# Kernel tuning notes

Hardware: AMD Instinct MI355X
Metric: run time of the kernel (lower is better)

## Reference

```python
import jax, jax.numpy as jnp
import numpy as np

COMMITMENT_COST = 0.25


def setup_inputs() -> dict:
    key = jax.random.key(0)
    k1, k2 = jax.random.split(key)
    inputs = jax.random.normal(k1, (32, 64, 32, 32), dtype=jnp.float32)  # (B, C, H, W)
    embed = jax.random.normal(k2, (64, 1024), dtype=jnp.float32)          # (embedding_dim, num_embeddings)
    return {"inputs": inputs, "embed": embed}


def reference(inputs, embed):
    # Eval-mode forward (EMA buffer updates are training-only side effects).
    B, C, H, W = inputs.shape
    K = embed.shape[1]
    flat = inputs.transpose(0, 2, 3, 1).reshape(-1, C)  # (N, C)
    N = flat.shape[0]

    distances = (jnp.sum(flat * flat, axis=1, keepdims=True)
                 + jnp.sum(embed * embed, axis=0)
                 - 2.0 * flat @ embed)
    encoding_indices = jnp.argmin(distances, axis=1)  # (N,)

    # Gather instead of one-hot @ embed.T (same math, no N x K one-hot)
    quantized = embed.T[encoding_indices]  # (N, C)

    e_latent_loss = jnp.mean((jax.lax.stop_gradient(quantized) - flat) ** 2)
    loss = COMMITMENT_COST * e_latent_loss

    # straight-through estimator
    quantized_st = flat + jax.lax.stop_gradient(quantized - flat)
    quantized_out = quantized_st.reshape(B, H, W, C).transpose(0, 3, 1, 2)

    # avg_probs via scatter-add counts (== mean of one-hot encodings)
    counts = jnp.zeros((K,), dtype=flat.dtype).at[encoding_indices].add(1.0)
    avg_probs = counts / N
    perplexity = jnp.exp(-jnp.sum(avg_probs * jnp.log(avg_probs + 1e-10)))

    return quantized_out, loss, encoding_indices, perplexity
```

## Files before the change

kernel.cpp:

```cpp
#include <hip/hip_runtime.h>

#define N_PIX  32768
#define C_DIM  64
#define K_EMB  1024
#define HW     1024
#define PIXB   32

#define OUT_Q_OFF    0
#define OUT_LOSS_OFF 2097152
#define OUT_IDX_OFF  2097153
#define OUT_PERP_OFF 2129921

typedef __attribute__((ext_vector_type(8)))  __bf16 bf16x8;
typedef __attribute__((ext_vector_type(16))) float  f32x16;

__device__ unsigned short g_esplit[3 * K_EMB * C_DIM];
__device__ uint4          g_eesplit[2 * K_EMB];
__device__ float          g_ee[K_EMB];
__device__ unsigned int   g_counts[K_EMB];
__device__ float          g_lossAcc;

__device__ __forceinline__ unsigned short f2bf(float f) {
    unsigned u = __float_as_uint(f);
    unsigned r = u + 0x7FFFu + ((u >> 16) & 1u);
    return (unsigned short)(r >> 16);
}
__device__ __forceinline__ float bf2f(unsigned short b) {
    return __uint_as_float(((unsigned)b) << 16);
}
__device__ __forceinline__ unsigned long long pack_score(float d, int k) {
    unsigned int u = __float_as_uint(d);
    u = (u & 0x80000000u) ? ~u : (u | 0x80000000u);
    return ((unsigned long long)u << 32) | (unsigned int)k;
}
__device__ __forceinline__ uint4 pack8(const unsigned short* v) {
    uint4 u;
    u.x = (unsigned)v[0] | ((unsigned)v[1] << 16);
    u.y = (unsigned)v[2] | ((unsigned)v[3] << 16);
    u.z = (unsigned)v[4] | ((unsigned)v[5] << 16);
    u.w = (unsigned)v[6] | ((unsigned)v[7] << 16);
    return u;
}
__device__ __forceinline__ unsigned long long shfl_xor32_u64(unsigned long long v) {
    unsigned lo = (unsigned)v, hi = (unsigned)(v >> 32);
    lo = __shfl_xor(lo, 32, 64);
    hi = __shfl_xor(hi, 32, 64);
    return ((unsigned long long)hi << 32) | lo;
}
#define UPD2(P1, P2, MM) { \
    if ((MM) < P1) { P2 = P1; P1 = (MM); } else if ((MM) < P2) P2 = (MM); }
#define MRG2(P1, P2, O1, O2) { \
    unsigned long long _lo = (O1) < P1 ? (O1) : P1; \
    unsigned long long _hi = (O1) < P1 ? P1 : (O1); \
    unsigned long long _m2 = (O2) < P2 ? (O2) : P2; \
    P1 = _lo; P2 = _hi < _m2 ? _hi : _m2; }

__global__ void k_prep(const float* __restrict__ embed) {
    const int code = blockIdx.x * 64 + threadIdx.x;
    if (code == 0) g_lossAcc = 0.f;
    g_counts[code] = 0u;
    const int tile = code >> 5, c32 = code & 31;
    uint4* o = reinterpret_cast<uint4*>(g_esplit);
    float ee = 0.f;
#pragma unroll
    for (int s = 0; s < 4; ++s)
#pragma unroll
        for (int hh = 0; hh < 2; ++hh) {
            unsigned short b1[8], b2[8], b3[8];
#pragma unroll
            for (int e = 0; e < 8; ++e) {
                const float x = embed[(s * 16 + hh * 8 + e) * K_EMB + code];
                ee = fmaf(x, x, ee);
                b1[e] = f2bf(x);
                const float r1 = x - bf2f(b1[e]);
                b2[e] = f2bf(r1);
                const float r2 = r1 - bf2f(b2[e]);
                b3[e] = f2bf(r2);
            }
            const int oi = tile * 256 + s * 64 + hh * 32 + c32;
            o[oi        ] = pack8(b1);
            o[oi +  8192] = pack8(b2);
            o[oi + 16384] = pack8(b3);
        }
    g_ee[code] = ee;
    const float v = -0.5f * ee;
    const unsigned short e1 = f2bf(v);
    const float r1 = v - bf2f(e1);
    const unsigned short e2 = f2bf(r1);
    const float r2 = r1 - bf2f(e2);
    const unsigned short e3 = f2bf(r2);
    g_eesplit[code] = make_uint4((unsigned)e1 | ((unsigned)e2 << 16),
                                 (unsigned)e3, 0u, 0u);
    g_eesplit[K_EMB + code] = make_uint4(0u, 0u, 0u, 0u);
}

__global__ __launch_bounds__(256, 2) void k_main(
    const float* __restrict__ inp, const float* __restrict__ embed,
    float* __restrict__ out_q, float* __restrict__ out_idx) {

    __shared__ float x_raw[C_DIM * PIXB];
    __shared__ uint4 xfrag[3 * 4 * 2 * PIXB];
    __shared__ unsigned long long red1[4][PIXB];
    __shared__ unsigned long long red2[4][PIXB];
    __shared__ int   ksel[PIXB];
    __shared__ float lred[4];
    __shared__ float bdist;

    const int tid = threadIdx.x;
    const int n0  = blockIdx.x * PIXB;
    const int b   = n0 >> 10;
    const int hw0 = n0 & 1023;
    const float* __restrict__ xg = inp + b * (C_DIM * HW) + hw0;

#pragma unroll
    for (int i = 0; i < 2; ++i) {
        const int F = tid + i * 256;
        const int c = F >> 3, p4 = (F & 7) << 2;
        *reinterpret_cast<float4*>(&x_raw[F << 2]) =
            *reinterpret_cast<const float4*>(xg + c * HW + p4);
    }
    __syncthreads();

    float sx2 = 0.f;
    {
        const int s = tid >> 6, hh = (tid >> 5) & 1, p = tid & 31;
        unsigned short b1[8], b2[8], b3[8];
#pragma unroll
        for (int e = 0; e < 8; ++e) {
            const float x = x_raw[(s * 16 + hh * 8 + e) * PIXB + p];
            sx2 = fmaf(x, x, sx2);
            b1[e] = f2bf(x);
            const float r1 = x - bf2f(b1[e]);
            b2[e] = f2bf(r1);
            const float r2 = r1 - bf2f(b2[e]);
            b3[e] = f2bf(r2);
        }
        const int fi = (s * 2 + hh) * PIXB + p;
        xfrag[fi            ] = pack8(b1);
        xfrag[fi + 8 * PIXB ] = pack8(b2);
        xfrag[fi + 16 * PIXB] = pack8(b3);
    }
    for (int off = 32; off; off >>= 1) sx2 += __shfl_down(sx2, off, 64);
    if ((tid & 63) == 0) lred[tid >> 6] = sx2;
    __syncthreads();

    const int w   = tid >> 6;
    const int ln  = tid & 63;
    const int c31 = ln & 31;
    const int h   = ln >> 5;
    const uint4* __restrict__ eg = reinterpret_cast<const uint4*>(g_esplit);
    const int abase = h * 32 + c31;
    const int pbase = c31;

    unsigned long long p1a = ~0ull, p2a = ~0ull;
    const uint4 bones = make_uint4(h ? 0u : 0x3F803F80u, h ? 0u : 0x00003F80u, 0u, 0u);

#define MFMA1(AF, BF) \
    acc = __builtin_amdgcn_mfma_f32_32x32x16_bf16( \
        __builtin_bit_cast(bf16x8, AF), __builtin_bit_cast(bf16x8, BF), acc, 0, 0, 0);

#pragma unroll 1
    for (int r = 0; r < 8; ++r) {
        const int ct = r * 4 + w;
        const int b0 = ct * 256 + abase;
        const int cb = ct * 32;
        uint4 ae0[4], ae1[4], a2[4], aee;
#pragma unroll
        for (int s = 0; s < 4; ++s) {
            ae0[s] = eg[b0 + s * 64];
            ae1[s] = eg[b0 + 8192 + s * 64];
            a2[s]  = eg[b0 + 16384 + s * 64];
        }
        aee = g_eesplit[h * K_EMB + ct * 32 + c31];

        f32x16 acc = {};
        MFMA1(aee, bones)
        {
            uint4 bx[4];
#pragma unroll
            for (int s = 0; s < 4; ++s) bx[s] = xfrag[(s * 2 + h) * PIXB + pbase];
#pragma unroll
            for (int s = 0; s < 4; ++s) { MFMA1(ae0[s], bx[s]) }
#pragma unroll
            for (int s = 0; s < 4; ++s) { MFMA1(ae1[s], bx[s]) }
        }
        {
            uint4 bx[4];
#pragma unroll
            for (int s = 0; s < 4; ++s) bx[s] = xfrag[(8 + s * 2 + h) * PIXB + pbase];
#pragma unroll
            for (int s = 0; s < 4; ++s) { MFMA1(ae0[s], bx[s]) }
#pragma unroll
            for (int s = 0; s < 4; ++s) { MFMA1(ae1[s], bx[s]) }
        }
        {
            uint4 bx[4];
#pragma unroll
            for (int s = 0; s < 4; ++s) bx[s] = xfrag[(16 + s * 2 + h) * PIXB + pbase];
#pragma unroll
            for (int s = 0; s < 4; ++s) { MFMA1(ae0[s], bx[s]) }
        }
        {
            uint4 bx[4];
#pragma unroll
            for (int s = 0; s < 4; ++s) bx[s] = xfrag[(s * 2 + h) * PIXB + pbase];
#pragma unroll
            for (int s = 0; s < 4; ++s) { MFMA1(a2[s], bx[s]) }
        }
#pragma unroll
        for (int rg = 0; rg < 16; ++rg) {
            const unsigned long long mm =
                pack_score(-acc[rg], cb + (rg & 3) + 8 * (rg >> 2) + 4 * h);
            UPD2(p1a, p2a, mm)
        }
    }
#undef MFMA1

    {
        unsigned long long o1 = shfl_xor32_u64(p1a), o2 = shfl_xor32_u64(p2a);
        MRG2(p1a, p2a, o1, o2)
        if (ln < 32) { red1[w][ln] = p1a; red2[w][ln] = p2a; }
    }
    __syncthreads();

    if (tid < PIXB) {
        unsigned long long M1 = red1[0][tid], M2 = red2[0][tid];
#pragma unroll
        for (int wv = 1; wv < 4; ++wv) { MRG2(M1, M2, red1[wv][tid], red2[wv][tid]) }
        const int k1 = (int)(unsigned int)(M1 & 0xFFFFFFFFull);
        const int k2 = (int)(unsigned int)(M2 & 0xFFFFFFFFull);
        float d1 = 0.f, d2 = 0.f;
        const float* xcol = x_raw + tid;
#pragma unroll 8
        for (int c = 0; c < C_DIM; ++c) {
            const float xv = xcol[c * PIXB];
            d1 = fmaf(xv, embed[c * K_EMB + k1], d1);
            d2 = fmaf(xv, embed[c * K_EMB + k2], d2);
        }
        const float dist1 = fmaf(-2.f, d1, g_ee[k1]);
        const float dist2 = fmaf(-2.f, d2, g_ee[k2]);
        const unsigned long long s1 = pack_score(dist1, k1);
        const unsigned long long s2 = pack_score(dist2, k2);
        const int   k     = (s1 < s2) ? k1 : k2;
        const float distw = (s1 < s2) ? dist1 : dist2;
        ksel[tid] = k;
        out_idx[n0 + tid] = (float)k;
        atomicAdd(g_counts + k, 1u);
        float dist = distw;
        for (int off = 16; off; off >>= 1) dist += __shfl_down(dist, off, 32);
        if (tid == 0) bdist = dist;
    }
    __syncthreads();

#pragma unroll
    for (int i = 0; i < 2; ++i) {
        const int F = tid + i * 256;
        const int c = F >> 3, p0 = (F & 7) << 2;
        float* oq = out_q + b * (C_DIM * HW) + c * HW + hw0 + p0;
        const float* er = embed + c * K_EMB;
        float4 q;
        q.x = er[ksel[p0 + 0]];
        q.y = er[ksel[p0 + 1]];
        q.z = er[ksel[p0 + 2]];
        q.w = er[ksel[p0 + 3]];
        *reinterpret_cast<float4*>(oq) = q;
    }
    if (tid == 0)
        atomicAdd(&g_lossAcc, lred[0] + lred[1] + lred[2] + lred[3] + bdist);
}

__global__ __launch_bounds__(1024) void k_scalar(float* __restrict__ out_loss,
                                                 float* __restrict__ out_perp) {
    __shared__ float red[16];
    const int tid = threadIdx.x;
    float p = (float)g_counts[tid] * (1.0f / (float)N_PIX);
    float t = p * logf(p + 1e-10f);
    for (int off = 32; off; off >>= 1) t += __shfl_down(t, off, 64);
    if ((tid & 63) == 0) red[tid >> 6] = t;
    __syncthreads();
    if (tid == 0) {
        float s = 0.f;
#pragma unroll
        for (int i = 0; i < 16; ++i) s += red[i];
        *out_perp = expf(-s);
        *out_loss = 0.25f * g_lossAcc * (1.0f / (float)(N_PIX * C_DIM));
    }
}

extern "C" void kernel_launch(void* const* d_in, const int* in_sizes, int n_in,
                              void* d_out, int out_size, void* d_ws, size_t ws_size,
                              hipStream_t stream) {
    const float* inp   = (const float*)d_in[0];
    const float* embed = (const float*)d_in[1];
    float* out = (float*)d_out;

    k_prep<<<dim3(16), dim3(64), 0, stream>>>(embed);
    k_main<<<dim3(N_PIX / PIXB), dim3(256), 0, stream>>>(
        inp, embed, out + OUT_Q_OFF, out + OUT_IDX_OFF);
    k_scalar<<<dim3(1), dim3(1024), 0, stream>>>(out + OUT_LOSS_OFF,
                                                 out + OUT_PERP_OFF);
}
```

Baseline: 118.9 us.

## Prefetch codebook tiles, float-packed top-2 tracking, fuse scalar finalize into main kernel

Restructures the main distance loop so that the next codebook tile is prefetched into registers while the current one feeds the MFMAs. The x fragments stay register-resident and the operand roles are swapped. The 64-bit packed top-2 compare is replaced by per-register float max/med3 tracking, with the tile id stashed in low mantissa bits and a two-stage LDS candidate reduction. The separate perplexity/loss kernel is folded into a last-block-done epilogue via an atomic counter. Occupancy hint drops to one block per SIMD pair and LDS use grows, and truncating mantissa bits could alter tie-breaking, though top-2 rescoring in fp32 mitigates this.

```diff
diff --git a/kernel.cpp b/kernel.cpp
--- a/kernel.cpp
+++ b/kernel.cpp
@@ -19,6 +19,7 @@
 __device__ float          g_ee[K_EMB];
 __device__ unsigned int   g_counts[K_EMB];
 __device__ float          g_lossAcc;
+__device__ unsigned int   g_done;
 
 __device__ __forceinline__ unsigned short f2bf(float f) {
     unsigned u = __float_as_uint(f);
@@ -41,23 +42,13 @@
     u.w = (unsigned)v[6] | ((unsigned)v[7] << 16);
     return u;
 }
-__device__ __forceinline__ unsigned long long shfl_xor32_u64(unsigned long long v) {
-    unsigned lo = (unsigned)v, hi = (unsigned)(v >> 32);
-    lo = __shfl_xor(lo, 32, 64);
-    hi = __shfl_xor(hi, 32, 64);
-    return ((unsigned long long)hi << 32) | lo;
-}
-#define UPD2(P1, P2, MM) { \
-    if ((MM) < P1) { P2 = P1; P1 = (MM); } else if ((MM) < P2) P2 = (MM); }
-#define MRG2(P1, P2, O1, O2) { \
-    unsigned long long _lo = (O1) < P1 ? (O1) : P1; \
-    unsigned long long _hi = (O1) < P1 ? P1 : (O1); \
-    unsigned long long _m2 = (O2) < P2 ? (O2) : P2; \
-    P1 = _lo; P2 = _hi < _m2 ? _hi : _m2; }
+#define FUPD2(M1, K1, M2, K2, F, KK) { \
+    if ((F) > M1) { M2 = M1; K2 = K1; M1 = (F); K1 = (KK); } \
+    else if ((F) > M2) { M2 = (F); K2 = (KK); } }
 
 __global__ void k_prep(const float* __restrict__ embed) {
     const int code = blockIdx.x * 64 + threadIdx.x;
-    if (code == 0) g_lossAcc = 0.f;
+    if (code == 0) { g_lossAcc = 0.f; g_done = 0u; }
     g_counts[code] = 0u;
     const int tile = code >> 5, c32 = code & 31;
     uint4* o = reinterpret_cast<uint4*>(g_esplit);
@@ -94,17 +85,20 @@
     g_eesplit[K_EMB + code] = make_uint4(0u, 0u, 0u, 0u);
 }
 
-__global__ __launch_bounds__(256, 2) void k_main(
+__global__ __launch_bounds__(256, 1) void k_main(
     const float* __restrict__ inp, const float* __restrict__ embed,
-    float* __restrict__ out_q, float* __restrict__ out_idx) {
-
-    __shared__ float x_raw[C_DIM * PIXB];
-    __shared__ uint4 xfrag[3 * 4 * 2 * PIXB];
-    __shared__ unsigned long long red1[4][PIXB];
-    __shared__ unsigned long long red2[4][PIXB];
-    __shared__ int   ksel[PIXB];
-    __shared__ float lred[4];
-    __shared__ float bdist;
+    float* __restrict__ out_q, float* __restrict__ out_idx,
+    float* __restrict__ out_loss, float* __restrict__ out_perp) {
+
+    __shared__ float    x_raw[C_DIM * PIXB];
+    __shared__ uint4    xfrag[3 * 4 * 2 * PIXB];
+    __shared__ unsigned cand1[PIXB * 128];
+    __shared__ unsigned cand2[PIXB * 128];
+    __shared__ uint4    pxm[PIXB][8];
+    __shared__ int      ksel[PIXB];
+    __shared__ float    lred[4];
+    __shared__ float    bdist;
+    __shared__ unsigned lastFlag;
 
     const int tid = threadIdx.x;
     const int n0  = blockIdx.x * PIXB;
@@ -150,85 +144,99 @@
     const int h   = ln >> 5;
     const uint4* __restrict__ eg = reinterpret_cast<const uint4*>(g_esplit);
     const int abase = h * 32 + c31;
-    const int pbase = c31;
-
-    unsigned long long p1a = ~0ull, p2a = ~0ull;
     const uint4 bones = make_uint4(h ? 0u : 0x3F803F80u, h ? 0u : 0x00003F80u, 0u, 0u);
+
+#define LOADE(DST, DSTE, CT) { \
+    const int bb = (CT) * 256 + abase; \
+    _Pragma("unroll") for (int s = 0; s < 4; ++s) { \
+        DST[s]     = eg[bb + s * 64]; \
+        DST[4 + s] = eg[bb +  8192 + s * 64]; \
+        DST[8 + s] = eg[bb + 16384 + s * 64]; } \
+    DSTE = g_eesplit[h * K_EMB + (CT) * 32 + c31]; }
+
+    uint4 pA[12], pAe, pB[12], pBe;
+    LOADE(pA, pAe, w)
+
+    uint4 xa0[4], xa1[4], xa2[4];
+#pragma unroll
+    for (int s = 0; s < 4; ++s) {
+        xa0[s] = xfrag[(     s * 2 + h) * PIXB + c31];
+        xa1[s] = xfrag[( 8 + s * 2 + h) * PIXB + c31];
+        xa2[s] = xfrag[(16 + s * 2 + h) * PIXB + c31];
+    }
+
+    float m1[16], m2[16];
+#pragma unroll
+    for (int rg = 0; rg < 16; ++rg) { m1[rg] = -INFINITY; m2[rg] = -INFINITY; }
 
 #define MFMA1(AF, BF) \
     acc = __builtin_amdgcn_mfma_f32_32x32x16_bf16( \
         __builtin_bit_cast(bf16x8, AF), __builtin_bit_cast(bf16x8, BF), acc, 0, 0, 0);
 
+#define STEP(CUR, CURE, NXT, NXTE, R) { \
+    { const int rn = (R) < 7 ? (R) + 1 : 7; LOADE(NXT, NXTE, rn * 4 + w) } \
+    f32x16 acc = {}; \
+    MFMA1(bones, CURE) \
+    _Pragma("unroll") for (int s = 0; s < 4; ++s) { MFMA1(xa0[s], CUR[s]) }      \
+    _Pragma("unroll") for (int s = 0; s < 4; ++s) { MFMA1(xa1[s], CUR[s]) }      \
+    _Pragma("unroll") for (int s = 0; s < 4; ++s) { MFMA1(xa2[s], CUR[s]) }      \
+    _Pragma("unroll") for (int s = 0; s < 4; ++s) { MFMA1(xa0[s], CUR[4 + s]) }  \
+    _Pragma("unroll") for (int s = 0; s < 4; ++s) { MFMA1(xa1[s], CUR[4 + s]) }  \
+    _Pragma("unroll") for (int s = 0; s < 4; ++s) { MFMA1(xa0[s], CUR[8 + s]) }  \
+    _Pragma("unroll") for (int rg = 0; rg < 16; ++rg) { \
+        const unsigned cu = (__float_as_uint(acc[rg]) & 0xFFFFFFF8u) | (unsigned)(R); \
+        const float cf = __uint_as_float(cu); \
+        m2[rg] = __builtin_amdgcn_fmed3f(m1[rg], m2[rg], cf); \
+        m1[rg] = fmaxf(m1[rg], cf); \
+    } }
+
 #pragma unroll 1
-    for (int r = 0; r < 8; ++r) {
-        const int ct = r * 4 + w;
-        const int b0 = ct * 256 + abase;
-        const int cb = ct * 32;
-        uint4 ae0[4], ae1[4], a2[4], aee;
-#pragma unroll
-        for (int s = 0; s < 4; ++s) {
-            ae0[s] = eg[b0 + s * 64];
-            ae1[s] = eg[b0 + 8192 + s * 64];
-            a2[s]  = eg[b0 + 16384 + s * 64];
-        }
-        aee = g_eesplit[h * K_EMB + ct * 32 + c31];
-
-        f32x16 acc = {};
-        MFMA1(aee, bones)
-        {
-            uint4 bx[4];
-#pragma unroll
-            for (int s = 0; s < 4; ++s) bx[s] = xfrag[(s * 2 + h) * PIXB + pbase];
-#pragma unroll
-            for (int s = 0; s < 4; ++s) { MFMA1(ae0[s], bx[s]) }
-#pragma unroll
-            for (int s = 0; s < 4; ++s) { MFMA1(ae1[s], bx[s]) }
-        }
-        {
-            uint4 bx[4];
-#pragma unroll
-            for (int s = 0; s < 4; ++s) bx[s] = xfrag[(8 + s * 2 + h) * PIXB + pbase];
-#pragma unroll
-            for (int s = 0; s < 4; ++s) { MFMA1(ae0[s], bx[s]) }
-#pragma unroll
-            for (int s = 0; s < 4; ++s) { MFMA1(ae1[s], bx[s]) }
-        }
-        {
-            uint4 bx[4];
-#pragma unroll
-            for (int s = 0; s < 4; ++s) bx[s] = xfrag[(16 + s * 2 + h) * PIXB + pbase];
-#pragma unroll
-            for (int s = 0; s < 4; ++s) { MFMA1(ae0[s], bx[s]) }
-        }
-        {
-            uint4 bx[4];
-#pragma unroll
-            for (int s = 0; s < 4; ++s) bx[s] = xfrag[(s * 2 + h) * PIXB + pbase];
-#pragma unroll
-            for (int s = 0; s < 4; ++s) { MFMA1(a2[s], bx[s]) }
-        }
-#pragma unroll
-        for (int rg = 0; rg < 16; ++rg) {
-            const unsigned long long mm =
-                pack_score(-acc[rg], cb + (rg & 3) + 8 * (rg >> 2) + 4 * h);
-            UPD2(p1a, p2a, mm)
-        }
-    }
+    for (int rr = 0; rr < 4; ++rr) {
+        STEP(pA, pAe, pB, pBe, 2 * rr)
+        STEP(pB, pBe, pA, pAe, 2 * rr + 1)
+    }
+#undef STEP
 #undef MFMA1
+#undef LOADE
+
+#pragma unroll
+    for (int rg = 0; rg < 16; ++rg) {
+        const int px = (rg & 3) + 8 * (rg >> 2) + 4 * h;
+        cand1[px * 128 + w * 32 + c31] = __float_as_uint(m1[rg]);
+        cand2[px * 128 + w * 32 + c31] = __float_as_uint(m2[rg]);
+    }
+    __syncthreads();
 
     {
-        unsigned long long o1 = shfl_xor32_u64(p1a), o2 = shfl_xor32_u64(p2a);
-        MRG2(p1a, p2a, o1, o2)
-        if (ln < 32) { red1[w][ln] = p1a; red2[w][ln] = p2a; }
+        const int px = tid >> 3, sl = tid & 7;
+        const int base = px * 128 + sl * 16;
+        float a1 = -INFINITY, a2 = -INFINITY; int k1 = 0, k2 = 0;
+#pragma unroll
+        for (int i = 0; i < 16; ++i) {
+            const int idx = sl * 16 + i;
+            const int klo = (idx >> 5) * 32 + (idx & 31);
+            unsigned u = cand1[base + i];
+            int kk = (int)((u & 7u) * 128u) + klo;
+            float f = __uint_as_float(u);
+            FUPD2(a1, k1, a2, k2, f, kk)
+            u = cand2[base + i];
+            kk = (int)((u & 7u) * 128u) + klo;
+            f = __uint_as_float(u);
+            FUPD2(a1, k1, a2, k2, f, kk)
+        }
+        pxm[px][sl] = make_uint4(__float_as_uint(a1), (unsigned)k1,
+                                 __float_as_uint(a2), (unsigned)k2);
     }
     __syncthreads();
 
     if (tid < PIXB) {
-        unsigned long long M1 = red1[0][tid], M2 = red2[0][tid];
-#pragma unroll
-        for (int wv = 1; wv < 4; ++wv) { MRG2(M1, M2, red1[wv][tid], red2[wv][tid]) }
-        const int k1 = (int)(unsigned int)(M1 & 0xFFFFFFFFull);
-        const int k2 = (int)(unsigned int)(M2 & 0xFFFFFFFFull);
+        float a1 = -INFINITY, a2 = -INFINITY; int k1 = 0, k2 = 0;
+#pragma unroll
+        for (int sl = 0; sl < 8; ++sl) {
+            const uint4 v = pxm[tid][sl];
+            FUPD2(a1, k1, a2, k2, __uint_as_float(v.x), (int)v.y)
+            FUPD2(a1, k1, a2, k2, __uint_as_float(v.z), (int)v.w)
+        }
         float d1 = 0.f, d2 = 0.f;
         const float* xcol = x_raw + tid;
 #pragma unroll 8
@@ -265,25 +273,30 @@
         q.w = er[ksel[p0 + 3]];
         *reinterpret_cast<float4*>(oq) = q;
     }
-    if (tid == 0)
+
+    if (tid == 0) {
         atomicAdd(&g_lossAcc, lred[0] + lred[1] + lred[2] + lred[3] + bdist);
-}
-
-__global__ __launch_bounds__(1024) void k_scalar(float* __restrict__ out_loss,
-                                                 float* __restrict__ out_perp) {
-    __shared__ float red[16];
-    const int tid = threadIdx.x;
-    float p = (float)g_counts[tid] * (1.0f / (float)N_PIX);
-    float t = p * logf(p + 1e-10f);
-    for (int off = 32; off; off >>= 1) t += __shfl_down(t, off, 64);
-    if ((tid & 63) == 0) red[tid >> 6] = t;
-    __syncthreads();
-    if (tid == 0) {
-        float s = 0.f;
-#pragma unroll
-        for (int i = 0; i < 16; ++i) s += red[i];
-        *out_perp = expf(-s);
-        *out_loss = 0.25f * g_lossAcc * (1.0f / (float)(N_PIX * C_DIM));
+        __threadfence();
+        lastFlag = (atomicAdd(&g_done, 1u) == (unsigned)(gridDim.x - 1)) ? 1u : 0u;
+    }
+    __syncthreads();
+    if (lastFlag) {
+        float t = 0.f;
+#pragma unroll
+        for (int i = 0; i < 4; ++i) {
+            const unsigned c = atomicAdd(&g_counts[tid * 4 + i], 0u);
+            const float p = (float)c * (1.0f / (float)N_PIX);
+            t += p * logf(p + 1e-10f);
+        }
+        for (int off = 32; off; off >>= 1) t += __shfl_down(t, off, 64);
+        if (ln == 0) lred[w] = t;
+        __syncthreads();
+        if (tid == 0) {
+            const float s  = lred[0] + lred[1] + lred[2] + lred[3];
+            const float la = atomicAdd(&g_lossAcc, 0.f);
+            *out_perp = expf(-s);
+            *out_loss = 0.25f * la * (1.0f / (float)(N_PIX * C_DIM));
+        }
     }
 }
 
@@ -296,7 +309,6 @@
 
     k_prep<<<dim3(16), dim3(64), 0, stream>>>(embed);
     k_main<<<dim3(N_PIX / PIXB), dim3(256), 0, stream>>>(
-        inp, embed, out + OUT_Q_OFF, out + OUT_IDX_OFF);
-    k_scalar<<<dim3(1), dim3(1024), 0, stream>>>(out + OUT_LOSS_OFF,
-                                                 out + OUT_PERP_OFF);
-}
+        inp, embed, out + OUT_Q_OFF, out + OUT_IDX_OFF,
+        out + OUT_LOSS_OFF, out + OUT_PERP_OFF);
+}
```

Result: slower. 157.1 us (+32.1%).
